# Kernel optimization log

Hardware: AMD Instinct MI355X
Metric: run time of the kernel (lower is better)

## Reference

```python
import jax, jax.numpy as jnp
import numpy as np

B, N, D = 8, 256, 256
LN_EPS = 1e-5


def setup_inputs() -> dict:
    key = jax.random.key(0)
    ks = jax.random.split(key, 8)
    s1 = 1.0 / np.sqrt(2 * D)  # torch Linear init scale ~ U(-1/sqrt(fan_in), ...); use normal*scale
    s2 = 1.0 / np.sqrt(D)
    return {
        "patch_features": jax.random.normal(ks[0], (B, N, D), dtype=jnp.float32),
        # relation_transform: Linear(2D, D) -> ReLU -> Linear(D, 1)
        "W1": jax.random.normal(ks[1], (2 * D, D), dtype=jnp.float32) * s1,
        "b1": jax.random.normal(ks[2], (D,), dtype=jnp.float32) * s1,
        "W2": jax.random.normal(ks[3], (D, 1), dtype=jnp.float32) * s2,
        "b2": jax.random.normal(ks[4], (1,), dtype=jnp.float32) * s2,
        # context_projection: Linear(D, D) + LayerNorm(D)
        "Wp": jax.random.normal(ks[5], (D, D), dtype=jnp.float32) * s2,
        "bp": jax.random.normal(ks[6], (D,), dtype=jnp.float32) * s2,
        "ln_gamma": jnp.ones((D,), dtype=jnp.float32),
        "ln_beta": jnp.zeros((D,), dtype=jnp.float32),
    }


def reference(patch_features, W1, b1, W2, b2, Wp, bp, ln_gamma, ln_beta):
    x = patch_features  # [B, N, D]
    d = x.shape[-1]
    # cat([x_i, x_j]) @ W1 == x_i @ W1[:D] + x_j @ W1[D:]
    hi = jnp.einsum("bnd,de->bne", x, W1[:d])   # [B, N, D]
    hj = jnp.einsum("bmd,de->bme", x, W1[d:])   # [B, N, D]
    h = jax.nn.relu(hi[:, :, None, :] + hj[:, None, :, :] + b1)  # [B, N, N, D]
    scores = jnp.einsum("bnmd,do->bnm", h, W2) + b2[0]            # [B, N, N]
    # diagonal entries stay exactly 0 (original never fills i == j)
    eye = jnp.eye(scores.shape[1], dtype=bool)
    scores = jnp.where(eye[None, :, :], 0.0, scores)
    weights = jax.nn.softmax(scores, axis=2)                      # [B, N, N]
    ctx = jnp.einsum("bnm,bmd->bnd", weights, x)                  # [B, N, D]
    proj = jnp.einsum("bnd,de->bne", ctx, Wp) + bp
    mu = jnp.mean(proj, axis=-1, keepdims=True)
    var = jnp.mean(jnp.square(proj - mu), axis=-1, keepdims=True)
    ln = (proj - mu) * jax.lax.rsqrt(var + LN_EPS) * ln_gamma + ln_beta
    return x + ln
```

## Files before the change

kernel.cpp:

```cpp
#include <hip/hip_runtime.h>

#define LN_EPS 1e-5f

__device__ __forceinline__ float wred_max(float v) {
#pragma unroll
    for (int off = 32; off; off >>= 1) v = fmaxf(v, __shfl_xor(v, off, 64));
    return v;
}
__device__ __forceinline__ float wred_sum(float v) {
#pragma unroll
    for (int off = 32; off; off >>= 1) v += __shfl_xor(v, off, 64);
    return v;
}

__global__ __launch_bounds__(256) void k_gemm_hij(
    const float* __restrict__ x,
    const float* __restrict__ W1,
    const float* __restrict__ b1,
    float* __restrict__ hi_ws,
    float* __restrict__ hjT)
{
    __shared__ __align__(16) float xs[4][256];
    const int t = threadIdx.x;
    const int lane = t & 63, w = t >> 6;
    const int row0 = blockIdx.x * 4;

    ((float4*)xs)[t] = ((const float4*)(x + (size_t)row0 * 256))[t];
    __syncthreads();

    const int half = w >> 1;
    const int r0 = (w & 1) * 2;
    const float* Wb = W1 + (size_t)half * 65536 + 4 * lane;

    float a00 = 0.f, a01 = 0.f, a02 = 0.f, a03 = 0.f;
    float a10 = 0.f, a11 = 0.f, a12 = 0.f, a13 = 0.f;

#pragma unroll 2
    for (int k = 0; k < 256; k += 4) {
        float4 q0 = *(const float4*)(Wb + (size_t)(k + 0) * 256);
        float4 q1 = *(const float4*)(Wb + (size_t)(k + 1) * 256);
        float4 q2 = *(const float4*)(Wb + (size_t)(k + 2) * 256);
        float4 q3 = *(const float4*)(Wb + (size_t)(k + 3) * 256);
        float4 xa = *(const float4*)&xs[r0][k];
        float4 xb = *(const float4*)&xs[r0 + 1][k];
        a00 = fmaf(xa.x, q0.x, a00); a00 = fmaf(xa.y, q1.x, a00);
        a00 = fmaf(xa.z, q2.x, a00); a00 = fmaf(xa.w, q3.x, a00);
        a01 = fmaf(xa.x, q0.y, a01); a01 = fmaf(xa.y, q1.y, a01);
        a01 = fmaf(xa.z, q2.y, a01); a01 = fmaf(xa.w, q3.y, a01);
        a02 = fmaf(xa.x, q0.z, a02); a02 = fmaf(xa.y, q1.z, a02);
        a02 = fmaf(xa.z, q2.z, a02); a02 = fmaf(xa.w, q3.z, a02);
        a03 = fmaf(xa.x, q0.w, a03); a03 = fmaf(xa.y, q1.w, a03);
        a03 = fmaf(xa.z, q2.w, a03); a03 = fmaf(xa.w, q3.w, a03);
        a10 = fmaf(xb.x, q0.x, a10); a10 = fmaf(xb.y, q1.x, a10);
        a10 = fmaf(xb.z, q2.x, a10); a10 = fmaf(xb.w, q3.x, a10);
        a11 = fmaf(xb.x, q0.y, a11); a11 = fmaf(xb.y, q1.y, a11);
        a11 = fmaf(xb.z, q2.y, a11); a11 = fmaf(xb.w, q3.y, a11);
        a12 = fmaf(xb.x, q0.z, a12); a12 = fmaf(xb.y, q1.z, a12);
        a12 = fmaf(xb.z, q2.z, a12); a12 = fmaf(xb.w, q3.z, a12);
        a13 = fmaf(xb.x, q0.w, a13); a13 = fmaf(xb.y, q1.w, a13);
        a13 = fmaf(xb.z, q2.w, a13); a13 = fmaf(xb.w, q3.w, a13);
    }

    if (half == 0) {
        float4 b4 = *(const float4*)(b1 + 4 * lane);
        float4 o0 = make_float4(a00 + b4.x, a01 + b4.y, a02 + b4.z, a03 + b4.w);
        float4 o1 = make_float4(a10 + b4.x, a11 + b4.y, a12 + b4.z, a13 + b4.w);
        *(float4*)&hi_ws[(size_t)(row0 + r0 + 0) * 256 + 4 * lane] = o0;
        *(float4*)&hi_ws[(size_t)(row0 + r0 + 1) * 256 + 4 * lane] = o1;
    } else {
        const int b = row0 >> 8;
        const int m = (row0 & 255) + r0;
        float* base = hjT + (size_t)b * 65536 + (size_t)(4 * lane) * 256 + m;
        base[0 * 256 + 0] = a00; base[1 * 256 + 0] = a01;
        base[2 * 256 + 0] = a02; base[3 * 256 + 0] = a03;
        base[0 * 256 + 1] = a10; base[1 * 256 + 1] = a11;
        base[2 * 256 + 1] = a12; base[3 * 256 + 1] = a13;
    }
}

__global__ __launch_bounds__(256) void k_fused(
    const float* __restrict__ x,
    const float* __restrict__ hi_ws,
    const float* __restrict__ hjT,
    const float* __restrict__ W2, const float* __restrict__ b2,
    const float* __restrict__ Wp, const float* __restrict__ bp,
    const float* __restrict__ gma, const float* __restrict__ bta,
    float* __restrict__ out)
{
    const int t = threadIdx.x;
    const int lane = t & 63, w = t >> 6;
    const int bn0 = blockIdx.x * 4;
    const int b = bn0 >> 8, n0 = bn0 & 255;

    __shared__ __align__(16) float hi_s[4][256];
    __shared__ __align__(16) float w2_s[256];
    __shared__ __align__(16) float wt_s[4][256];
    __shared__ __align__(16) float ctx_s[4][256];
    __shared__ __align__(16) float sred[4][4][256];
    __shared__ float part[8][4];

#pragma unroll
    for (int i = 0; i < 4; i++) hi_s[i][t] = hi_ws[(size_t)(bn0 + i) * 256 + t];
    w2_s[t] = W2[t];
    __syncthreads();

    {
        const float* hjp = hjT + (size_t)b * 65536 + (size_t)(w * 64) * 256 + 4 * lane;
        float sp[4][4];
#pragma unroll
        for (int n = 0; n < 4; n++)
#pragma unroll
            for (int j = 0; j < 4; j++) sp[n][j] = 0.f;

#pragma unroll 2
        for (int dc = 0; dc < 64; dc += 4) {
            float4 h0 = *(const float4*)(hjp + (size_t)(dc + 0) * 256);
            float4 h1 = *(const float4*)(hjp + (size_t)(dc + 1) * 256);
            float4 h2 = *(const float4*)(hjp + (size_t)(dc + 2) * 256);
            float4 h3 = *(const float4*)(hjp + (size_t)(dc + 3) * 256);
            float4 wq = *(const float4*)&w2_s[w * 64 + dc];
#pragma unroll
            for (int n = 0; n < 4; n++) {
                float4 hi4 = *(const float4*)&hi_s[n][w * 64 + dc];
                sp[n][0] = fmaf(fmaxf(hi4.x + h0.x, 0.f), wq.x, sp[n][0]);
                sp[n][0] = fmaf(fmaxf(hi4.y + h1.x, 0.f), wq.y, sp[n][0]);
                sp[n][0] = fmaf(fmaxf(hi4.z + h2.x, 0.f), wq.z, sp[n][0]);
                sp[n][0] = fmaf(fmaxf(hi4.w + h3.x, 0.f), wq.w, sp[n][0]);
                sp[n][1] = fmaf(fmaxf(hi4.x + h0.y, 0.f), wq.x, sp[n][1]);
                sp[n][1] = fmaf(fmaxf(hi4.y + h1.y, 0.f), wq.y, sp[n][1]);
                sp[n][1] = fmaf(fmaxf(hi4.z + h2.y, 0.f), wq.z, sp[n][1]);
                sp[n][1] = fmaf(fmaxf(hi4.w + h3.y, 0.f), wq.w, sp[n][1]);
                sp[n][2] = fmaf(fmaxf(hi4.x + h0.z, 0.f), wq.x, sp[n][2]);
                sp[n][2] = fmaf(fmaxf(hi4.y + h1.z, 0.f), wq.y, sp[n][2]);
                sp[n][2] = fmaf(fmaxf(hi4.z + h2.z, 0.f), wq.z, sp[n][2]);
                sp[n][2] = fmaf(fmaxf(hi4.w + h3.z, 0.f), wq.w, sp[n][2]);
                sp[n][3] = fmaf(fmaxf(hi4.x + h0.w, 0.f), wq.x, sp[n][3]);
                sp[n][3] = fmaf(fmaxf(hi4.y + h1.w, 0.f), wq.y, sp[n][3]);
                sp[n][3] = fmaf(fmaxf(hi4.z + h2.w, 0.f), wq.z, sp[n][3]);
                sp[n][3] = fmaf(fmaxf(hi4.w + h3.w, 0.f), wq.w, sp[n][3]);
            }
        }
#pragma unroll
        for (int n = 0; n < 4; n++)
            *(float4*)&sred[w][n][4 * lane] =
                make_float4(sp[n][0], sp[n][1], sp[n][2], sp[n][3]);
    }
    __syncthreads();

    float b2v = b2[0];
    float s[4];
#pragma unroll
    for (int i = 0; i < 4; i++) {
        s[i] = ((sred[0][i][t] + sred[1][i][t]) +
                (sred[2][i][t] + sred[3][i][t])) + b2v;
        if (t == n0 + i) s[i] = 0.f;
    }
#pragma unroll
    for (int i = 0; i < 4; i++) {
        float m = wred_max(s[i]);
        if (lane == 0) part[i][w] = m;
    }
    __syncthreads();
    float ev[4];
#pragma unroll
    for (int i = 0; i < 4; i++) {
        float mx = fmaxf(fmaxf(part[i][0], part[i][1]),
                         fmaxf(part[i][2], part[i][3]));
        ev[i] = __expf(s[i] - mx);
        float sm = wred_sum(ev[i]);
        if (lane == 0) part[4 + i][w] = sm;
    }
    __syncthreads();
#pragma unroll
    for (int i = 0; i < 4; i++) {
        float tot = (part[4 + i][0] + part[4 + i][1]) +
                    (part[4 + i][2] + part[4 + i][3]);
        wt_s[i][t] = ev[i] / tot;
    }
    __syncthreads();

    {
        const float* xpp = x + (size_t)b * 65536 + (size_t)(w * 64) * 256 + 4 * lane;
        float cp[4][4];
#pragma unroll
        for (int n = 0; n < 4; n++)
#pragma unroll
            for (int j = 0; j < 4; j++) cp[n][j] = 0.f;

#pragma unroll 2
        for (int mc = 0; mc < 64; mc += 4) {
            float4 x0 = *(const float4*)(xpp + (size_t)(mc + 0) * 256);
            float4 x1 = *(const float4*)(xpp + (size_t)(mc + 1) * 256);
            float4 x2 = *(const float4*)(xpp + (size_t)(mc + 2) * 256);
            float4 x3 = *(const float4*)(xpp + (size_t)(mc + 3) * 256);
#pragma unroll
            for (int n = 0; n < 4; n++) {
                float4 wt4 = *(const float4*)&wt_s[n][w * 64 + mc];
                cp[n][0] = fmaf(wt4.x, x0.x, cp[n][0]);
                cp[n][0] = fmaf(wt4.y, x1.x, cp[n][0]);
                cp[n][0] = fmaf(wt4.z, x2.x, cp[n][0]);
                cp[n][0] = fmaf(wt4.w, x3.x, cp[n][0]);
                cp[n][1] = fmaf(wt4.x, x0.y, cp[n][1]);
                cp[n][1] = fmaf(wt4.y, x1.y, cp[n][1]);
                cp[n][1] = fmaf(wt4.z, x2.y, cp[n][1]);
                cp[n][1] = fmaf(wt4.w, x3.y, cp[n][1]);
                cp[n][2] = fmaf(wt4.x, x0.z, cp[n][2]);
                cp[n][2] = fmaf(wt4.y, x1.z, cp[n][2]);
                cp[n][2] = fmaf(wt4.z, x2.z, cp[n][2]);
                cp[n][2] = fmaf(wt4.w, x3.z, cp[n][2]);
                cp[n][3] = fmaf(wt4.x, x0.w, cp[n][3]);
                cp[n][3] = fmaf(wt4.y, x1.w, cp[n][3]);
                cp[n][3] = fmaf(wt4.z, x2.w, cp[n][3]);
                cp[n][3] = fmaf(wt4.w, x3.w, cp[n][3]);
            }
        }
#pragma unroll
        for (int n = 0; n < 4; n++)
            *(float4*)&sred[w][n][4 * lane] =
                make_float4(cp[n][0], cp[n][1], cp[n][2], cp[n][3]);
    }
    __syncthreads();
#pragma unroll
    for (int i = 0; i < 4; i++)
        ctx_s[i][t] = (sred[0][i][t] + sred[1][i][t]) +
                      (sred[2][i][t] + sred[3][i][t]);
    __syncthreads();

    {
        const float* wpp = Wp + (size_t)(w * 64) * 256 + 4 * lane;
        float pq[4][4];
#pragma unroll
        for (int n = 0; n < 4; n++)
#pragma unroll
            for (int j = 0; j < 4; j++) pq[n][j] = 0.f;

#pragma unroll 2
        for (int dc = 0; dc < 64; dc += 4) {
            float4 q0 = *(const float4*)(wpp + (size_t)(dc + 0) * 256);
            float4 q1 = *(const float4*)(wpp + (size_t)(dc + 1) * 256);
            float4 q2 = *(const float4*)(wpp + (size_t)(dc + 2) * 256);
            float4 q3 = *(const float4*)(wpp + (size_t)(dc + 3) * 256);
#pragma unroll
            for (int n = 0; n < 4; n++) {
                float4 c4 = *(const float4*)&ctx_s[n][w * 64 + dc];
                pq[n][0] = fmaf(c4.x, q0.x, pq[n][0]);
                pq[n][0] = fmaf(c4.y, q1.x, pq[n][0]);
                pq[n][0] = fmaf(c4.z, q2.x, pq[n][0]);
                pq[n][0] = fmaf(c4.w, q3.x, pq[n][0]);
                pq[n][1] = fmaf(c4.x, q0.y, pq[n][1]);
                pq[n][1] = fmaf(c4.y, q1.y, pq[n][1]);
                pq[n][1] = fmaf(c4.z, q2.y, pq[n][1]);
                pq[n][1] = fmaf(c4.w, q3.y, pq[n][1]);
                pq[n][2] = fmaf(c4.x, q0.z, pq[n][2]);
                pq[n][2] = fmaf(c4.y, q1.z, pq[n][2]);
                pq[n][2] = fmaf(c4.z, q2.z, pq[n][2]);
                pq[n][2] = fmaf(c4.w, q3.z, pq[n][2]);
                pq[n][3] = fmaf(c4.x, q0.w, pq[n][3]);
                pq[n][3] = fmaf(c4.y, q1.w, pq[n][3]);
                pq[n][3] = fmaf(c4.z, q2.w, pq[n][3]);
                pq[n][3] = fmaf(c4.w, q3.w, pq[n][3]);
            }
        }
#pragma unroll
        for (int n = 0; n < 4; n++)
            *(float4*)&sred[w][n][4 * lane] =
                make_float4(pq[n][0], pq[n][1], pq[n][2], pq[n][3]);
    }
    __syncthreads();

    float bpv = bp[t];
    float p[4];
#pragma unroll
    for (int i = 0; i < 4; i++)
        p[i] = ((sred[0][i][t] + sred[1][i][t]) +
                (sred[2][i][t] + sred[3][i][t])) + bpv;

#pragma unroll
    for (int i = 0; i < 4; i++) {
        float su = wred_sum(p[i]);
        float sq = wred_sum(p[i] * p[i]);
        if (lane == 0) { part[i][w] = su; part[4 + i][w] = sq; }
    }
    __syncthreads();
    float gv = gma[t], bv = bta[t];
#pragma unroll
    for (int i = 0; i < 4; i++) {
        float su = (part[i][0] + part[i][1]) + (part[i][2] + part[i][3]);
        float sq = (part[4 + i][0] + part[4 + i][1]) +
                   (part[4 + i][2] + part[4 + i][3]);
        float mu = su * (1.f / 256.f);
        float var = sq * (1.f / 256.f) - mu * mu;
        float ln = (p[i] - mu) * rsqrtf(var + LN_EPS) * gv + bv;
        out[(size_t)(bn0 + i) * 256 + t] = x[(size_t)(bn0 + i) * 256 + t] + ln;
    }
}

extern "C" void kernel_launch(void* const* d_in, const int* in_sizes, int n_in,
                              void* d_out, int out_size, void* d_ws, size_t ws_size,
                              hipStream_t stream) {
    const float* x   = (const float*)d_in[0];
    const float* W1  = (const float*)d_in[1];
    const float* b1  = (const float*)d_in[2];
    const float* W2  = (const float*)d_in[3];
    const float* b2  = (const float*)d_in[4];
    const float* Wp  = (const float*)d_in[5];
    const float* bp  = (const float*)d_in[6];
    const float* gma = (const float*)d_in[7];
    const float* bta = (const float*)d_in[8];
    float* out = (float*)d_out;

    float* hi_ws = (float*)d_ws;
    float* hjT   = hi_ws + (size_t)2048 * 256;

    k_gemm_hij<<<512, 256, 0, stream>>>(x, W1, b1, hi_ws, hjT);
    k_fused<<<512, 256, 0, stream>>>(x, hi_ws, hjT, W2, b2, Wp, bp,
                                     gma, bta, out);
}
```

Before: 113.4 us.

## Enlarge hij GEMM row tile, vectorize hjT stores, interleave fused-block batch order

The first GEMM now handles 8 rows per block (4 per wave) instead of 4, so each W1 float4 load is reused across twice as many rows and the grid is halved. The transposed hjT writes become float4 stores of four consecutive m values instead of scalar strided stores. The fused kernel remaps blockIdx so consecutive blocks cycle across batches, which changes how blocks touch hjT and x per batch in the caches. Inner loops are unrolled 4 instead of 2, adding register pressure. Fewer blocks in the first kernel lowers parallelism on a large GPU.

```diff
diff --git a/kernel.cpp b/kernel.cpp
--- a/kernel.cpp
+++ b/kernel.cpp
@@ -20,20 +20,24 @@
     float* __restrict__ hi_ws,
     float* __restrict__ hjT)
 {
-    __shared__ __align__(16) float xs[4][256];
+    __shared__ __align__(16) float xs[8][256];
     const int t = threadIdx.x;
     const int lane = t & 63, w = t >> 6;
-    const int row0 = blockIdx.x * 4;
-
-    ((float4*)xs)[t] = ((const float4*)(x + (size_t)row0 * 256))[t];
+    const int row0 = blockIdx.x * 8;
+
+    ((float4*)xs)[t]       = ((const float4*)(x + (size_t)row0 * 256))[t];
+    ((float4*)xs)[t + 256] = ((const float4*)(x + (size_t)row0 * 256))[t + 256];
     __syncthreads();
 
     const int half = w >> 1;
-    const int r0 = (w & 1) * 2;
+    const int r0 = (w & 1) * 4;
     const float* Wb = W1 + (size_t)half * 65536 + 4 * lane;
 
-    float a00 = 0.f, a01 = 0.f, a02 = 0.f, a03 = 0.f;
-    float a10 = 0.f, a11 = 0.f, a12 = 0.f, a13 = 0.f;
+    float acc[4][4];
+#pragma unroll
+    for (int r = 0; r < 4; r++)
+#pragma unroll
+        for (int c = 0; c < 4; c++) acc[r][c] = 0.f;
 
 #pragma unroll 2
     for (int k = 0; k < 256; k += 4) {
@@ -41,40 +45,44 @@
         float4 q1 = *(const float4*)(Wb + (size_t)(k + 1) * 256);
         float4 q2 = *(const float4*)(Wb + (size_t)(k + 2) * 256);
         float4 q3 = *(const float4*)(Wb + (size_t)(k + 3) * 256);
-        float4 xa = *(const float4*)&xs[r0][k];
-        float4 xb = *(const float4*)&xs[r0 + 1][k];
-        a00 = fmaf(xa.x, q0.x, a00); a00 = fmaf(xa.y, q1.x, a00);
-        a00 = fmaf(xa.z, q2.x, a00); a00 = fmaf(xa.w, q3.x, a00);
-        a01 = fmaf(xa.x, q0.y, a01); a01 = fmaf(xa.y, q1.y, a01);
-        a01 = fmaf(xa.z, q2.y, a01); a01 = fmaf(xa.w, q3.y, a01);
-        a02 = fmaf(xa.x, q0.z, a02); a02 = fmaf(xa.y, q1.z, a02);
-        a02 = fmaf(xa.z, q2.z, a02); a02 = fmaf(xa.w, q3.z, a02);
-        a03 = fmaf(xa.x, q0.w, a03); a03 = fmaf(xa.y, q1.w, a03);
-        a03 = fmaf(xa.z, q2.w, a03); a03 = fmaf(xa.w, q3.w, a03);
-        a10 = fmaf(xb.x, q0.x, a10); a10 = fmaf(xb.y, q1.x, a10);
-        a10 = fmaf(xb.z, q2.x, a10); a10 = fmaf(xb.w, q3.x, a10);
-        a11 = fmaf(xb.x, q0.y, a11); a11 = fmaf(xb.y, q1.y, a11);
-        a11 = fmaf(xb.z, q2.y, a11); a11 = fmaf(xb.w, q3.y, a11);
-        a12 = fmaf(xb.x, q0.z, a12); a12 = fmaf(xb.y, q1.z, a12);
-        a12 = fmaf(xb.z, q2.z, a12); a12 = fmaf(xb.w, q3.z, a12);
-        a13 = fmaf(xb.x, q0.w, a13); a13 = fmaf(xb.y, q1.w, a13);
-        a13 = fmaf(xb.z, q2.w, a13); a13 = fmaf(xb.w, q3.w, a13);
+#pragma unroll
+        for (int r = 0; r < 4; r++) {
+            float4 xr = *(const float4*)&xs[r0 + r][k];
+            acc[r][0] = fmaf(xr.x, q0.x, acc[r][0]);
+            acc[r][0] = fmaf(xr.y, q1.x, acc[r][0]);
+            acc[r][0] = fmaf(xr.z, q2.x, acc[r][0]);
+            acc[r][0] = fmaf(xr.w, q3.x, acc[r][0]);
+            acc[r][1] = fmaf(xr.x, q0.y, acc[r][1]);
+            acc[r][1] = fmaf(xr.y, q1.y, acc[r][1]);
+            acc[r][1] = fmaf(xr.z, q2.y, acc[r][1]);
+            acc[r][1] = fmaf(xr.w, q3.y, acc[r][1]);
+            acc[r][2] = fmaf(xr.x, q0.z, acc[r][2]);
+            acc[r][2] = fmaf(xr.y, q1.z, acc[r][2]);
+            acc[r][2] = fmaf(xr.z, q2.z, acc[r][2]);
+            acc[r][2] = fmaf(xr.w, q3.z, acc[r][2]);
+            acc[r][3] = fmaf(xr.x, q0.w, acc[r][3]);
+            acc[r][3] = fmaf(xr.y, q1.w, acc[r][3]);
+            acc[r][3] = fmaf(xr.z, q2.w, acc[r][3]);
+            acc[r][3] = fmaf(xr.w, q3.w, acc[r][3]);
+        }
     }
 
     if (half == 0) {
         float4 b4 = *(const float4*)(b1 + 4 * lane);
-        float4 o0 = make_float4(a00 + b4.x, a01 + b4.y, a02 + b4.z, a03 + b4.w);
-        float4 o1 = make_float4(a10 + b4.x, a11 + b4.y, a12 + b4.z, a13 + b4.w);
-        *(float4*)&hi_ws[(size_t)(row0 + r0 + 0) * 256 + 4 * lane] = o0;
-        *(float4*)&hi_ws[(size_t)(row0 + r0 + 1) * 256 + 4 * lane] = o1;
+#pragma unroll
+        for (int r = 0; r < 4; r++) {
+            float4 o = make_float4(acc[r][0] + b4.x, acc[r][1] + b4.y,
+                                   acc[r][2] + b4.z, acc[r][3] + b4.w);
+            *(float4*)&hi_ws[(size_t)(row0 + r0 + r) * 256 + 4 * lane] = o;
+        }
     } else {
         const int b = row0 >> 8;
-        const int m = (row0 & 255) + r0;
-        float* base = hjT + (size_t)b * 65536 + (size_t)(4 * lane) * 256 + m;
-        base[0 * 256 + 0] = a00; base[1 * 256 + 0] = a01;
-        base[2 * 256 + 0] = a02; base[3 * 256 + 0] = a03;
-        base[0 * 256 + 1] = a10; base[1 * 256 + 1] = a11;
-        base[2 * 256 + 1] = a12; base[3 * 256 + 1] = a13;
+        const int m0 = (row0 & 255) + r0;
+#pragma unroll
+        for (int e = 0; e < 4; e++) {
+            float4 v = make_float4(acc[0][e], acc[1][e], acc[2][e], acc[3][e]);
+            *(float4*)&hjT[(size_t)b * 65536 + (size_t)(4 * lane + e) * 256 + m0] = v;
+        }
     }
 }
 
@@ -89,8 +97,9 @@
 {
     const int t = threadIdx.x;
     const int lane = t & 63, w = t >> 6;
-    const int bn0 = blockIdx.x * 4;
-    const int b = bn0 >> 8, n0 = bn0 & 255;
+    const int b = blockIdx.x & 7;
+    const int n0 = (blockIdx.x >> 3) * 4;
+    const int bn0 = b * 256 + n0;
 
     __shared__ __align__(16) float hi_s[4][256];
     __shared__ __align__(16) float w2_s[256];
@@ -112,7 +121,7 @@
 #pragma unroll
             for (int j = 0; j < 4; j++) sp[n][j] = 0.f;
 
-#pragma unroll 2
+#pragma unroll 4
         for (int dc = 0; dc < 64; dc += 4) {
             float4 h0 = *(const float4*)(hjp + (size_t)(dc + 0) * 256);
             float4 h1 = *(const float4*)(hjp + (size_t)(dc + 1) * 256);
@@ -187,7 +196,7 @@
 #pragma unroll
             for (int j = 0; j < 4; j++) cp[n][j] = 0.f;
 
-#pragma unroll 2
+#pragma unroll 4
         for (int mc = 0; mc < 64; mc += 4) {
             float4 x0 = *(const float4*)(xpp + (size_t)(mc + 0) * 256);
             float4 x1 = *(const float4*)(xpp + (size_t)(mc + 1) * 256);
@@ -234,7 +243,7 @@
 #pragma unroll
             for (int j = 0; j < 4; j++) pq[n][j] = 0.f;
 
-#pragma unroll 2
+#pragma unroll 4
         for (int dc = 0; dc < 64; dc += 4) {
             float4 q0 = *(const float4*)(wpp + (size_t)(dc + 0) * 256);
             float4 q1 = *(const float4*)(wpp + (size_t)(dc + 1) * 256);
@@ -312,7 +321,7 @@
     float* hi_ws = (float*)d_ws;
     float* hjT   = hi_ws + (size_t)2048 * 256;
 
-    k_gemm_hij<<<512, 256, 0, stream>>>(x, W1, b1, hi_ws, hjT);
+    k_gemm_hij<<<256, 256, 0, stream>>>(x, W1, b1, hi_ws, hjT);
     k_fused<<<512, 256, 0, stream>>>(x, hi_ws, hjT, W2, b2, Wp, bp,
                                      gma, bta, out);
 }
```

Result: slower. 128.4 us (+13.2%).
